# Kernel optimization log

Measured on AMD Instinct MI355X. Metric: run time of the kernel, lower is better.

Reference implementation:

```python
import jax, jax.numpy as jnp
import numpy as np

BETA = 0.001

def setup_inputs() -> dict:
    key = jax.random.key(0)
    y_samples = jax.random.normal(key, (1024, 256), dtype=jnp.float32)
    return {"y_samples": y_samples}

def reference(y_samples):
    # diff[i, j, d] = y[j, d] - y[i, d]  -> mean over j (dim=1)
    # negative[i, d] = -mean_j (y_j - y_i)^2 / 2 ; positive = 0
    diff = y_samples[None, :, :] - y_samples[:, None, :]  # [N, N, D]
    negative = -jnp.mean(diff * diff, axis=1) / 2.0        # [N, D]
    mi = jnp.mean(-jnp.sum(negative, axis=-1))             # scalar
    return mi * BETA
```

## Files before the change

kernel.cpp:

```cpp
#include <hip/hip_runtime.h>


#define N_ROWS 1024
#define D 256
#define NBLK 16
#define ROWS_PER_BLK (N_ROWS / NBLK)
#define BETA 0.001f
#define MAGIC 0x9E3779B97F4A7C15ULL

__global__ __launch_bounds__(256)
void club_onepass(const float* __restrict__ y,
                  float* __restrict__ ws,
                  float* __restrict__ out) {
    const int d = threadIdx.x;
    const int b = blockIdx.x;
    unsigned long long* flags =
        (unsigned long long*)(ws + NBLK * 2 * D);

    {
        const float* p = y + (size_t)b * ROWS_PER_BLK * D + d;
        float s = 0.f, s2 = 0.f;
#pragma unroll 16
        for (int r = 0; r < ROWS_PER_BLK; ++r) {
            float v = p[(size_t)r * D];
            s  += v;
            s2 += v * v;
        }
        ws[b * (2 * D) + d]     = s;
        ws[b * (2 * D) + D + d] = s2;
    }

    if (b != 0) {
        __threadfence();
        __syncthreads();
        if (threadIdx.x == 0)
            __hip_atomic_store(&flags[b], (unsigned long long)MAGIC,
                               __ATOMIC_RELEASE, __HIP_MEMORY_SCOPE_AGENT);
        return;
    }

    if (threadIdx.x >= 1 && threadIdx.x < NBLK) {
        while (__hip_atomic_load(&flags[threadIdx.x], __ATOMIC_ACQUIRE,
                                 __HIP_MEMORY_SCOPE_AGENT) != MAGIC) { }
    }
    __syncthreads();
    __threadfence();

    float S = 0.f, S2 = 0.f;
#pragma unroll
    for (int g = 0; g < NBLK; ++g) {
        S  += ws[g * (2 * D) + d];
        S2 += ws[g * (2 * D) + D + d];
    }
    const float invN = 1.0f / (float)N_ROWS;
    float mu = S * invN;
    float v  = S2 * invN - mu * mu;

#pragma unroll
    for (int off = 32; off > 0; off >>= 1)
        v += __shfl_down(v, off, 64);

    __shared__ float lds[4];
    const int wave = threadIdx.x >> 6;
    const int lane = threadIdx.x & 63;
    if (lane == 0) lds[wave] = v;
    __syncthreads();
    if (threadIdx.x == 0) {
        float t = lds[0] + lds[1] + lds[2] + lds[3];
        out[0] = t * BETA;
    }
}

extern "C" void kernel_launch(void* const* d_in, const int* in_sizes, int n_in,
                              void* d_out, int out_size, void* d_ws, size_t ws_size,
                              hipStream_t stream) {
    const float* y = (const float*)d_in[0];
    float* ws = (float*)d_ws;
    float* out = (float*)d_out;

    club_onepass<<<NBLK, D, 0, stream>>>(y, ws, out);
}
```

Before: 56.72 us.

## Spread column-sum pass over 64 blocks with float4 loads and LDS reduction

Raises the block count from 16 to 64 so each block reads only 16 rows. Each thread now loads float4 vectors: four row-groups per block each cover the 256 columns, and the partial sums are combined through shared memory. The final reduction in block 0 is also vectorised across four row-groups. This spreads the memory-bound reading phase across more CUs and widens each load. In exchange, block 0 must wait on four times as many flags and reduce four times as many partials.

After: 63.60 us. 1.12x slower.

```diff
diff --git a/kernel.cpp b/kernel.cpp
--- a/kernel.cpp
+++ b/kernel.cpp
@@ -3,7 +3,7 @@
 
 #define N_ROWS 1024
 #define D 256
-#define NBLK 16
+#define NBLK 64
 #define ROWS_PER_BLK (N_ROWS / NBLK)
 #define BETA 0.001f
 #define MAGIC 0x9E3779B97F4A7C15ULL
@@ -12,62 +12,88 @@
 void club_onepass(const float* __restrict__ y,
                   float* __restrict__ ws,
                   float* __restrict__ out) {
-    const int d = threadIdx.x;
-    const int b = blockIdx.x;
+    const int t  = threadIdx.x;
+    const int b  = blockIdx.x;
+    const int c  = t & 63;
+    const int rg = t >> 6;
     unsigned long long* flags =
         (unsigned long long*)(ws + NBLK * 2 * D);
 
+    __shared__ float4 lsum[256];
+    __shared__ float4 lsq[256];
+
+    float4 S = {0.f, 0.f, 0.f, 0.f};
+    float4 Q = {0.f, 0.f, 0.f, 0.f};
     {
-        const float* p = y + (size_t)b * ROWS_PER_BLK * D + d;
-        float s = 0.f, s2 = 0.f;
-#pragma unroll 16
-        for (int r = 0; r < ROWS_PER_BLK; ++r) {
-            float v = p[(size_t)r * D];
-            s  += v;
-            s2 += v * v;
+        const float4* yp = (const float4*)(y + (size_t)b * ROWS_PER_BLK * D);
+#pragma unroll
+        for (int r = 0; r < 4; ++r) {
+            float4 v = yp[(rg * 4 + r) * (D / 4) + c];
+            S.x += v.x; S.y += v.y; S.z += v.z; S.w += v.w;
+            Q.x += v.x * v.x; Q.y += v.y * v.y;
+            Q.z += v.z * v.z; Q.w += v.w * v.w;
         }
-        ws[b * (2 * D) + d]     = s;
-        ws[b * (2 * D) + D + d] = s2;
+    }
+    lsum[t] = S; lsq[t] = Q;
+    __syncthreads();
+
+    if (t < 64) {
+        float4 a0 = lsum[t], a1 = lsum[t + 64], a2 = lsum[t + 128], a3 = lsum[t + 192];
+        float4 q0 = lsq[t],  q1 = lsq[t + 64],  q2 = lsq[t + 128],  q3 = lsq[t + 192];
+        float4 Ss = {a0.x + a1.x + a2.x + a3.x, a0.y + a1.y + a2.y + a3.y,
+                     a0.z + a1.z + a2.z + a3.z, a0.w + a1.w + a2.w + a3.w};
+        float4 Qs = {q0.x + q1.x + q2.x + q3.x, q0.y + q1.y + q2.y + q3.y,
+                     q0.z + q1.z + q2.z + q3.z, q0.w + q1.w + q2.w + q3.w};
+        ((float4*)(ws + (size_t)b * 2 * D))[c]            = Ss;
+        ((float4*)(ws + (size_t)b * 2 * D))[D / 4 + c]    = Qs;
     }
 
     if (b != 0) {
         __threadfence();
         __syncthreads();
-        if (threadIdx.x == 0)
+        if (t == 0)
             __hip_atomic_store(&flags[b], (unsigned long long)MAGIC,
                                __ATOMIC_RELEASE, __HIP_MEMORY_SCOPE_AGENT);
         return;
     }
 
-    if (threadIdx.x >= 1 && threadIdx.x < NBLK) {
-        while (__hip_atomic_load(&flags[threadIdx.x], __ATOMIC_ACQUIRE,
+    if (t >= 1 && t < NBLK) {
+        while (__hip_atomic_load(&flags[t], __ATOMIC_ACQUIRE,
                                  __HIP_MEMORY_SCOPE_AGENT) != MAGIC) { }
     }
     __syncthreads();
     __threadfence();
 
-    float S = 0.f, S2 = 0.f;
-#pragma unroll
-    for (int g = 0; g < NBLK; ++g) {
-        S  += ws[g * (2 * D) + d];
-        S2 += ws[g * (2 * D) + D + d];
+    float4 FS = {0.f, 0.f, 0.f, 0.f};
+    float4 FQ = {0.f, 0.f, 0.f, 0.f};
+    for (int g = rg; g < NBLK; g += 4) {
+        const float4* ps = (const float4*)(ws + (size_t)g * 2 * D);
+        float4 a = ps[c];
+        float4 q = ps[D / 4 + c];
+        FS.x += a.x; FS.y += a.y; FS.z += a.z; FS.w += a.w;
+        FQ.x += q.x; FQ.y += q.y; FQ.z += q.z; FQ.w += q.w;
     }
-    const float invN = 1.0f / (float)N_ROWS;
-    float mu = S * invN;
-    float v  = S2 * invN - mu * mu;
+    lsum[t] = FS; lsq[t] = FQ;
+    __syncthreads();
+
+    if (t < 64) {
+        float4 a0 = lsum[t], a1 = lsum[t + 64], a2 = lsum[t + 128], a3 = lsum[t + 192];
+        float4 q0 = lsq[t],  q1 = lsq[t + 64],  q2 = lsq[t + 128],  q3 = lsq[t + 192];
+        float4 Ss = {a0.x + a1.x + a2.x + a3.x, a0.y + a1.y + a2.y + a3.y,
+                     a0.z + a1.z + a2.z + a3.z, a0.w + a1.w + a2.w + a3.w};
+        float4 Qs = {q0.x + q1.x + q2.x + q3.x, q0.y + q1.y + q2.y + q3.y,
+                     q0.z + q1.z + q2.z + q3.z, q0.w + q1.w + q2.w + q3.w};
+        const float invN = 1.0f / (float)N_ROWS;
+        float4 mu  = {Ss.x * invN, Ss.y * invN, Ss.z * invN, Ss.w * invN};
+        float4 var = {Qs.x * invN - mu.x * mu.x, Qs.y * invN - mu.y * mu.y,
+                      Qs.z * invN - mu.z * mu.z, Qs.w * invN - mu.w * mu.w};
+        float v = var.x + var.y + var.z + var.w;
 
 #pragma unroll
-    for (int off = 32; off > 0; off >>= 1)
-        v += __shfl_down(v, off, 64);
+        for (int off = 32; off > 0; off >>= 1)
+            v += __shfl_down(v, off, 64);
 
-    __shared__ float lds[4];
-    const int wave = threadIdx.x >> 6;
-    const int lane = threadIdx.x & 63;
-    if (lane == 0) lds[wave] = v;
-    __syncthreads();
-    if (threadIdx.x == 0) {
-        float t = lds[0] + lds[1] + lds[2] + lds[3];
-        out[0] = t * BETA;
+        if (t == 0) out[0] = v * BETA;
     }
 }
 
```
